# Kernel optimization log

Measured on AMD Instinct MI355X. Metric: run time of the kernel, lower is better.

## Reference

```python
import jax, jax.numpy as jnp
import numpy as np

DN = ('NCHW', 'OIHW', 'NCHW')
WINDOW_SIZES = (11, 25, 49)


def conv(x, w, b=None, pad=0, groups=1):
    y = jax.lax.conv_general_dilated(
        x, w, window_strides=(1, 1), padding=((pad, pad), (pad, pad)),
        dimension_numbers=DN, feature_group_count=groups)
    if b is not None:
        y = y + b[None, :, None, None]
    return y


def box_mean(f, wsize):
    # depthwise box-filter local mean with reflect padding (matches F.pad mode='reflect')
    C = f.shape[1]
    p = wsize // 2
    fp = jnp.pad(f, ((0, 0), (0, 0), (p, p), (p, p)), mode='reflect')
    k = jnp.ones((C, 1, wsize, wsize), f.dtype) / (wsize * wsize)
    return conv(fp, k, groups=C)


def std_map(features, wsize):
    # per-channel local std, channel-weighted sum, then **0.8
    C = features.shape[1]
    # C == 8 here, so weights are softmax(ones) == uniform (torch path for C != 4)
    cw = jax.nn.softmax(jnp.ones((C,), features.dtype))
    m = box_mean(features, wsize)
    m2 = box_mean(features ** 2, wsize)
    var = jnp.clip(m2 - m ** 2, 1e-6, None)
    res = jnp.sum(cw[None, :, None, None] * jnp.sqrt(var), axis=1, keepdims=True)
    return res ** 0.8  # [B,1,H,W]


def setup_inputs() -> dict:
    key = jax.random.key(0)
    ks = jax.random.split(key, 8)
    B, C, H, W = 8, 4, 512, 512
    x = jax.random.normal(ks[0], (B, C, H, W), dtype=jnp.float32)
    conv1_w = jax.random.normal(ks[1], (32, 4, 3, 3), dtype=jnp.float32) * 0.1
    conv1_b = jnp.zeros((32,), jnp.float32)
    conv2_w = jax.random.normal(ks[2], (16, 32, 3, 3), dtype=jnp.float32) * 0.05
    conv2_b = jnp.zeros((16,), jnp.float32)
    conv3_w = jax.random.normal(ks[3], (8, 16, 3, 3), dtype=jnp.float32) * 0.05
    conv3_b = jnp.zeros((8,), jnp.float32)
    # scale_fusion init: weight = 1/len(window_sizes), bias = 0
    fusion_w = jnp.full((1, len(WINDOW_SIZES), 1, 1), 1.0 / len(WINDOW_SIZES), jnp.float32)
    fusion_b = jnp.zeros((1,), jnp.float32)
    channel_weights = jnp.ones((4,), jnp.float32) / 4.0
    return dict(x=x, conv1_w=conv1_w, conv1_b=conv1_b, conv2_w=conv2_w,
                conv2_b=conv2_b, conv3_w=conv3_w, conv3_b=conv3_b,
                fusion_w=fusion_w, fusion_b=fusion_b,
                channel_weights=channel_weights)


def reference(x, conv1_w, conv1_b, conv2_w, conv2_b, conv3_w, conv3_b,
              fusion_w, fusion_b, channel_weights):
    lrelu = lambda v: jnp.where(v >= 0, v, 0.2 * v)
    # feature extractor: conv3x3 -> lrelu -> conv3x3 -> lrelu -> conv3x3
    f = lrelu(conv(x, conv1_w, conv1_b, pad=1))
    f = lrelu(conv(f, conv2_w, conv2_b, pad=1))
    f = conv(f, conv3_w, conv3_b, pad=1)  # [B,8,H,W]
    # multi-scale std maps
    maps = [std_map(f, w) for w in WINDOW_SIZES]
    multi = jnp.concatenate(maps, axis=1)  # [B,3,H,W]
    fused = jax.nn.relu(conv(multi, fusion_w, fusion_b, pad=0))  # [B,1,H,W]
    # adaptive thresholds (global quantiles over the whole fused std map)
    qs = jnp.quantile(fused.reshape(-1), jnp.array([0.25, 0.75], fused.dtype))
    q25, q75 = qs[0], qs[1]
    iqr = q75 - q25
    gstd = jnp.std(x, axis=(2, 3), keepdims=True, ddof=1)  # [B,4,1,1] (torch unbiased)
    lo = (q25 - 0.5 * iqr) * jnp.ones_like(gstd)
    hi = (q75 + 0.5 * iqr) * jnp.ones_like(gstd)
    gf = jnp.clip(gstd * 5.0, 0.5, 2.0)
    lo, hi = lo * gf, hi * gf
    cw = jax.nn.softmax(channel_weights)[None, :, None, None]
    cstd = jnp.std(x * cw, axis=(2, 3), keepdims=True, ddof=1)
    cf = jnp.clip(cstd * 2.0, 0.8, 1.2)
    lo, hi = lo * cf, hi * cf
    # mask generation: broadcast [B,1,H,W] vs [B,4,1,1] -> [B,4,H,W], then mean over C
    n = jnp.clip((fused - lo) / (hi - lo), 0.0, 1.0)
    mask = jax.nn.sigmoid(6.0 * n - 3.0)
    return jnp.mean(mask, axis=1, keepdims=True)  # [B,1,H,W]
```

## Files before the change

kernel.cpp:

```cpp
#include <hip/hip_runtime.h>
#include <cmath>

#define HH 512
#define WW 512
#define NB 8
#define CIN 4
#define C2 32
#define C3 16
#define CF 8
#define HW (HH*WW)
#define NPIX (NB*HW)
#define NBC 2

#define SEGC 10
#define SW   320
#define SVW  ((SW + (SW>>4) + 3) | 1)
#define RSW  (256 + 16 + 2)

__device__ __forceinline__ float lrelu_f(float v){ return v < 0.f ? 0.2f*v : v; }
__device__ __forceinline__ int reflect_i(int i){ int r = i < 0 ? -i : i; return r >= HH ? 2*HH - 2 - r : r; }
__device__ __forceinline__ int swz(int j){ return j + (j >> 4); }

template<int Ci, int Co, bool LRELU>
__global__ __launch_bounds__(256) void k_conv8(const float* __restrict__ in,
                                               const float* __restrict__ wgt,
                                               const float* __restrict__ bias,
                                               float* __restrict__ outp)
{
    constexpr int NG = Co/8;
    __shared__ float wl[NG*Ci*72];
    __shared__ float bl[Co];
    for (int i = threadIdx.x; i < Co*Ci*9; i += 256){
        int g  = i / (Ci*72);
        int r  = i - g*(Ci*72);
        int ci = r / 72;
        int q  = r - ci*72;
        int tap = q >> 3, ocl = q & 7;
        wl[i] = wgt[((g*8 + ocl)*Ci + ci)*9 + tap];
    }
    if (threadIdx.x < Co) bl[threadIdx.x] = bias[threadIdx.x];
    __syncthreads();

    int bid   = blockIdx.x;
    int local = bid % (NG*128);
    int b     = bid / (NG*128);
    int cb    = local & 3;
    int rb    = (local >> 2) & 31;
    int cg    = local >> 7;
    int tid   = threadIdx.x;
    int lane  = tid & 31;
    int col   = cb*128 + lane*4;
    int row0  = rb*16  + (tid >> 5)*2;
    int co0   = cg*8;
    const float* inb = in + (size_t)b*Ci*HW;

    float acc[8][2][4];
    #pragma unroll
    for (int j=0;j<8;j++){
        float bv = bl[co0+j];
        #pragma unroll
        for (int r=0;r<2;r++)
            #pragma unroll
            for (int p=0;p<4;p++) acc[j][r][p] = bv;
    }

    #pragma unroll 1
    for (int ci=0; ci<Ci; ci++){
        float v[4][6];
        const float* inc = inb + (size_t)ci*HW;
        #pragma unroll
        for (int dy=0;dy<4;dy++){
            int hh = row0 + dy - 1;
            int hc = hh < 0 ? 0 : (hh > HH-1 ? HH-1 : hh);
            bool hok = (unsigned)hh < (unsigned)HH;
            const float* rowp = inc + hc*WW;
            float4 m  = *(const float4*)(rowp + col);
            float  v0 = (col > 0)      ? rowp[col-1] : 0.f;
            float  v5 = (col+4 < WW)   ? rowp[col+4] : 0.f;
            if (!hok){ m.x=0.f; m.y=0.f; m.z=0.f; m.w=0.f; v0=0.f; v5=0.f; }
            v[dy][0]=v0; v[dy][1]=m.x; v[dy][2]=m.y;
            v[dy][3]=m.z; v[dy][4]=m.w; v[dy][5]=v5;
        }
        const float* wp = &wl[(cg*Ci + ci)*72];
        #pragma unroll
        for (int t=0;t<9;t++){
            int dy = t/3, dx = t - 3*(t/3);
            float w8[8];
            #pragma unroll
            for (int o=0;o<8;o++) w8[o] = wp[t*8 + o];
            #pragma unroll
            for (int o=0;o<8;o++)
                #pragma unroll
                for (int r=0;r<2;r++)
                    #pragma unroll
                    for (int p=0;p<4;p++)
                        acc[o][r][p] = fmaf(v[dy+r][dx+p], w8[o], acc[o][r][p]);
        }
    }

    float* ob = outp + (size_t)b*Co*HW;
    #pragma unroll
    for (int j=0;j<8;j++){
        #pragma unroll
        for (int r=0;r<2;r++){
            float4 o;
            o.x = LRELU ? lrelu_f(acc[j][r][0]) : acc[j][r][0];
            o.y = LRELU ? lrelu_f(acc[j][r][1]) : acc[j][r][1];
            o.z = LRELU ? lrelu_f(acc[j][r][2]) : acc[j][r][2];
            o.w = LRELU ? lrelu_f(acc[j][r][3]) : acc[j][r][3];
            *(float4*)(ob + (size_t)(co0+j)*HW + (size_t)(row0+r)*WW + col) = o;
        }
    }
}

template<int WS>
__device__ __forceinline__ float scale_step(float2* __restrict__ svq,
                                            float* __restrict__ resv,
                                            const float* vs, const float* vq,
                                            float fws)
{
    constexpr int P   = WS/2;
    constexpr int OFF = 24 - P;
    constexpr float inv = 1.f/((float)WS*(float)WS);
    const int tid = threadIdx.x;
    const int ch  = tid >> 5;
    const int seg = tid & 31;

    __syncthreads();
    #pragma unroll
    for (int k=0;k<SEGC;k++){
        int j = k*32 + seg;
        svq[ch*SVW + swz(j)] = make_float2(vs[k], vq[k]);
    }
    __syncthreads();

    int base = OFF + seg*8;
    float S = 0.f, Q = 0.f;
    #pragma unroll
    for (int q=0;q<WS;q++){
        float2 t = svq[ch*SVW + swz(base+q)];
        S += t.x; Q += t.y;
    }
    float res[8];
    #pragma unroll
    for (int t8=0;t8<8;t8++){
        float m = S*inv, m2 = Q*inv;
        res[t8] = sqrtf(fmaxf(fmaf(-m, m, m2), 1e-6f));
        if (t8 < 7){
            float2 ta = svq[ch*SVW + swz(base+t8+WS)];
            float2 tb = svq[ch*SVW + swz(base+t8)];
            S += ta.x - tb.x; Q += ta.y - tb.y;
        }
    }
    #pragma unroll
    for (int t8=0;t8<8;t8++)
        resv[ch*RSW + swz(seg*8+t8)] = res[t8];
    __syncthreads();

    float a = 0.f;
    #pragma unroll
    for (int cc=0;cc<CF;cc++) a += resv[cc*RSW + swz(tid)];
    return fws * powf(a*0.125f, 0.8f);
}

__global__ __launch_bounds__(256) void k_std3(const float* __restrict__ f,
                                              float* __restrict__ fused,
                                              const float* __restrict__ fwv)
{
    __shared__ float2 svq[CF*SVW];
    __shared__ float  resv[CF*RSW];

    int bid  = blockIdx.x;
    int band = bid & 31;
    int half = (bid >> 5) & 1;
    int b    = bid >> 6;
    int r0   = band*16;
    int c0   = half*256;
    int tid  = threadIdx.x;
    int ch   = tid >> 5;
    int seg  = tid & 31;
    const float* fp = f + (size_t)(b*CF + ch)*HW;

    int rc[SEGC];
    #pragma unroll
    for (int k=0;k<SEGC;k++){
        int gc = c0 - 24 + k*32 + seg;
        gc = gc < 0 ? -gc : (gc > WW-1 ? 2*WW-2 - gc : gc);
        rc[k] = gc;
    }

    float vs49[SEGC], vq49[SEGC], vs25[SEGC], vq25[SEGC], vs11[SEGC], vq11[SEGC];
    #pragma unroll
    for (int k=0;k<SEGC;k++){
        vs49[k]=0.f; vq49[k]=0.f; vs25[k]=0.f; vq25[k]=0.f; vs11[k]=0.f; vq11[k]=0.f;
    }
    #pragma unroll 1
    for (int dy=-24; dy<=24; dy++){
        const float* rp = fp + (size_t)reflect_i(r0+dy)*WW;
        bool in25 = (dy >= -12 && dy <= 12);
        bool in11 = (dy >= -5  && dy <= 5);
        #pragma unroll
        for (int k=0;k<SEGC;k++){
            float v = rp[rc[k]]; float v2 = v*v;
            vs49[k] += v; vq49[k] += v2;
            if (in25){ vs25[k] += v; vq25[k] += v2; }
            if (in11){ vs11[k] += v; vq11[k] += v2; }
        }
    }

    float fw0 = fwv[0], fw1 = fwv[1], fw2 = fwv[2];

    for (int rr=0; rr<16; rr++){
        int r = r0 + rr;
        float val;
        val  = scale_step<11>(svq, resv, vs11, vq11, fw0);
        val += scale_step<25>(svq, resv, vs25, vq25, fw1);
        val += scale_step<49>(svq, resv, vs49, vq49, fw2);
        fused[((size_t)b*HH + r)*WW + c0 + tid] = val;
        if (rr < 15){
            {   const float* ep = fp + (size_t)reflect_i(r+25)*WW;
                const float* lp = fp + (size_t)reflect_i(r-24)*WW;
                #pragma unroll
                for (int k=0;k<SEGC;k++){
                    float e = ep[rc[k]], l = lp[rc[k]];
                    vs49[k] += e - l;
                    vq49[k] = fmaf(e, e, vq49[k]); vq49[k] = fmaf(-l, l, vq49[k]);
                }
            }
            {   const float* ep = fp + (size_t)reflect_i(r+13)*WW;
                const float* lp = fp + (size_t)reflect_i(r-12)*WW;
                #pragma unroll
                for (int k=0;k<SEGC;k++){
                    float e = ep[rc[k]], l = lp[rc[k]];
                    vs25[k] += e - l;
                    vq25[k] = fmaf(e, e, vq25[k]); vq25[k] = fmaf(-l, l, vq25[k]);
                }
            }
            {   const float* ep = fp + (size_t)reflect_i(r+6)*WW;
                const float* lp = fp + (size_t)reflect_i(r-5)*WW;
                #pragma unroll
                for (int k=0;k<SEGC;k++){
                    float e = ep[rc[k]], l = lp[rc[k]];
                    vs11[k] += e - l;
                    vq11[k] = fmaf(e, e, vq11[k]); vq11[k] = fmaf(-l, l, vq11[k]);
                }
            }
        }
    }
}

__global__ void k_h8(const float* __restrict__ fused, const float* __restrict__ fb,
                     unsigned* __restrict__ hist8)
{
    __shared__ unsigned lh[256];
    lh[threadIdx.x] = 0;
    __syncthreads();
    float fbv = fb[0];
    int i = blockIdx.x*256 + threadIdx.x;
    int stride = gridDim.x*256;
    for (; i < NPIX; i += stride){
        float v = fmaxf(fused[i] + fbv, 0.f);
        atomicAdd(&lh[__float_as_uint(v) >> 24], 1u);
    }
    __syncthreads();
    if (lh[threadIdx.x]) atomicAdd(&hist8[threadIdx.x], lh[threadIdx.x]);
}

__global__ void k_scan8(const unsigned* __restrict__ hist8,
                        int* __restrict__ cand8, int* __restrict__ rank8)
{
    if (threadIdx.x == 0){
        const unsigned RK[4] = {524287u, 524288u, 1572863u, 1572864u};
        unsigned cum = 0; int qi = 0;
        for (int b = 0; b < 256 && qi < 4; b++){
            unsigned cnt = hist8[b];
            while (qi < 4 && RK[qi] < cum + cnt){
                cand8[qi] = b; rank8[qi] = (int)(RK[qi] - cum); qi++;
            }
            cum += cnt;
        }
    }
}

__global__ void k_h8b(const float* __restrict__ fused, const float* __restrict__ fb,
                      const int* __restrict__ cand8, unsigned* __restrict__ hist8b)
{
    __shared__ unsigned lh[1024];
    for (int i = threadIdx.x; i < 1024; i += 256) lh[i] = 0;
    __syncthreads();
    float fbv = fb[0];
    int c0 = cand8[0], c1 = cand8[1], c2 = cand8[2], c3 = cand8[3];
    bool d1 = (c1 != c0);
    bool d2 = (c2 != c0) && (c2 != c1);
    bool d3 = (c3 != c0) && (c3 != c1) && (c3 != c2);
    int i = blockIdx.x*256 + threadIdx.x;
    int stride = gridDim.x*256;
    for (; i < NPIX; i += stride){
        unsigned u = __float_as_uint(fmaxf(fused[i] + fbv, 0.f));
        int hi = (int)(u >> 24);
        unsigned mid = (u >> 16) & 0xffu;
        if (hi == c0)       atomicAdd(&lh[mid],       1u);
        if (d1 && hi == c1) atomicAdd(&lh[256u+mid],  1u);
        if (d2 && hi == c2) atomicAdd(&lh[512u+mid],  1u);
        if (d3 && hi == c3) atomicAdd(&lh[768u+mid],  1u);
    }
    __syncthreads();
    for (int i = threadIdx.x; i < 1024; i += 256)
        if (lh[i]) atomicAdd(&hist8b[i], lh[i]);
}

__global__ void k_scan8b(const unsigned* __restrict__ hist8b,
                         const int* __restrict__ cand8, const int* __restrict__ rank8,
                         int* __restrict__ cand16, int* __restrict__ rank16)
{
    int qi = threadIdx.x;
    if (qi < 4){
        int slot = qi;
        for (int j = 0; j < qi; j++) if (cand8[j] == cand8[qi]){ slot = j; break; }
        const unsigned* h = hist8b + slot*256;
        unsigned k = (unsigned)rank8[qi], cum = 0;
        for (int b = 0; b < 256; b++){
            unsigned cnt = h[b];
            if (cnt && k >= cum && k < cum + cnt){
                cand16[qi] = (cand8[qi] << 8) | b;
                rank16[qi] = (int)(k - cum);
            }
            cum += cnt;
        }
    }
}

__global__ void k_h16(const float* __restrict__ fused, const float* __restrict__ fb,
                      const int* __restrict__ cand16, unsigned* __restrict__ histlo)
{
    float fbv = fb[0];
    int c0 = cand16[0], c1 = cand16[1], c2 = cand16[2], c3 = cand16[3];
    bool d1 = (c1 != c0);
    bool d2 = (c2 != c0) && (c2 != c1);
    bool d3 = (c3 != c0) && (c3 != c1) && (c3 != c2);
    int i = blockIdx.x*256 + threadIdx.x;
    int stride = gridDim.x*256;
    for (; i < NPIX; i += stride){
        unsigned u = __float_as_uint(fmaxf(fused[i] + fbv, 0.f));
        int hi = (int)(u >> 16);
        unsigned lo = u & 0xffffu;
        if (hi == c0)       atomicAdd(&histlo[lo],           1u);
        if (d1 && hi == c1) atomicAdd(&histlo[65536u + lo],  1u);
        if (d2 && hi == c2) atomicAdd(&histlo[131072u + lo], 1u);
        if (d3 && hi == c3) atomicAdd(&histlo[196608u + lo], 1u);
    }
}

__global__ void k_scan16(const unsigned* __restrict__ histlo,
                         const int* __restrict__ cand16, const int* __restrict__ rank16,
                         float* __restrict__ ostat)
{
    int qi = blockIdx.x;
    int slot = qi;
    for (int j = 0; j < qi; j++) if (cand16[j] == cand16[qi]){ slot = j; break; }
    const unsigned* hist = histlo + (size_t)slot*65536;
    __shared__ unsigned csum[256];
    __shared__ unsigned cbase[256];
    int t = threadIdx.x;
    unsigned s = 0;
    for (int i = 0; i < 256; i++) s += hist[t*256 + i];
    csum[t] = s;
    __syncthreads();
    if (t == 0){ unsigned run = 0; for (int i = 0; i < 256; i++){ cbase[i] = run; run += csum[i]; } }
    __syncthreads();
    unsigned k = (unsigned)rank16[qi];
    unsigned cum = cbase[t];
    for (int i = 0; i < 256; i++){
        unsigned cnt = hist[t*256 + i];
        if (cnt && k >= cum && k < cum + cnt)
            ostat[qi] = __uint_as_float(((unsigned)cand16[qi] << 16) | (unsigned)(t*256 + i));
        cum += cnt;
    }
}

__global__ void k_gstd_part(const float* __restrict__ x, double* __restrict__ part)
{
    int bid = blockIdx.x;
    int plane = bid >> 3, chunk = bid & 7;
    const float4* p4 = (const float4*)(x + (size_t)plane*HW + (size_t)chunk*32768);
    int t = threadIdx.x;
    double s=0.0, s2=0.0;
    for (int k=0;k<32;k++){
        float4 v = p4[k*256 + t];
        s  += (double)v.x + (double)v.y + (double)v.z + (double)v.w;
        s2 += (double)v.x*v.x + (double)v.y*v.y + (double)v.z*v.z + (double)v.w*v.w;
    }
    __shared__ double rs[256], rq[256];
    rs[t]=s; rq[t]=s2; __syncthreads();
    for (int off=128; off>0; off>>=1){
        if (t<off){ rs[t]+=rs[t+off]; rq[t]+=rq[t+off]; }
        __syncthreads();
    }
    if (t==0){ part[bid*2]=rs[0]; part[bid*2+1]=rq[0]; }
}

__global__ void k_gstd_final(const double* __restrict__ part, float* __restrict__ gstd)
{
    int t = threadIdx.x;
    if (t < 32){
        double s=0.0, s2=0.0;
        for (int j=0;j<8;j++){ s += part[(t*8+j)*2]; s2 += part[(t*8+j)*2+1]; }
        const double N = 262144.0;
        double var = (s2 - s*s/N) / (N - 1.0);
        gstd[t] = (float)sqrt(var < 0.0 ? 0.0 : var);
    }
}

__global__ void k_finalize(const float* __restrict__ ostat, const float* __restrict__ gstd,
                           const float* __restrict__ cwin, float* __restrict__ lov, float* __restrict__ hiv)
{
    int t = threadIdx.x;
    if (t < 32){
        float q25 = ostat[0] + 0.75f*(ostat[1]-ostat[0]);
        float q75 = ostat[2] + 0.25f*(ostat[3]-ostat[2]);
        float iqr = q75 - q25;
        float lo_b = q25 - 0.5f*iqr, hi_b = q75 + 0.5f*iqr;
        int c = t & 3;
        float m = fmaxf(fmaxf(cwin[0],cwin[1]), fmaxf(cwin[2],cwin[3]));
        float e0 = expf(cwin[0]-m), e1 = expf(cwin[1]-m), e2 = expf(cwin[2]-m), e3 = expf(cwin[3]-m);
        float smc = expf(cwin[c]-m) / (e0+e1+e2+e3);
        float g  = gstd[t];
        float gf = fminf(fmaxf(g*5.f, 0.5f), 2.f);
        float cf = fminf(fmaxf(smc*g*2.f, 0.8f), 1.2f);
        lov[t] = lo_b*gf*cf;
        hiv[t] = hi_b*gf*cf;
    }
}

__global__ void k_mask(const float* __restrict__ fused_in, const float* __restrict__ fb,
                       const float* __restrict__ lov, const float* __restrict__ hiv,
                       float* __restrict__ outp)
{
    int i = blockIdx.x*256 + threadIdx.x;
    float F = fmaxf(fused_in[i] + fb[0], 0.f);
    int b = i >> 18;
    float o = 0.f;
    #pragma unroll
    for (int c=0;c<4;c++){
        float lo = lov[b*4+c], hi = hiv[b*4+c];
        float n = (F - lo) / (hi - lo);
        n = fminf(fmaxf(n, 0.f), 1.f);
        o += 1.f/(1.f + expf(3.f - 6.f*n));
    }
    outp[i] = 0.25f * o;
}

extern "C" void kernel_launch(void* const* d_in, const int* in_sizes, int n_in,
                              void* d_out, int out_size, void* d_ws, size_t ws_size,
                              hipStream_t stream)
{
    const float* x  = (const float*)d_in[0];
    const float* w1 = (const float*)d_in[1];
    const float* b1 = (const float*)d_in[2];
    const float* w2 = (const float*)d_in[3];
    const float* b2 = (const float*)d_in[4];
    const float* w3 = (const float*)d_in[5];
    const float* b3 = (const float*)d_in[6];
    const float* fw = (const float*)d_in[7];
    const float* fb = (const float*)d_in[8];
    const float* cw = (const float*)d_in[9];
    float* out = (float*)d_out;
    char* ws = (char*)d_ws;

    size_t off = 0;
    auto take = [&](size_t bytes)->size_t{ size_t o = off; off += (bytes + 255) & ~(size_t)255; return o; };
    size_t o_h8     = take(256*4);
    size_t o_h8b    = take(1024*4);
    size_t o_histlo = take((size_t)4*65536*4);
    size_t o_c8     = take(4*4);
    size_t o_r8     = take(4*4);
    size_t o_c16    = take(4*4);
    size_t o_r16    = take(4*4);
    size_t o_os     = take(4*4);
    size_t o_part   = take(512*8);
    size_t o_gs     = take(32*4);
    size_t o_lo     = take(32*4);
    size_t o_hi     = take(32*4);
    size_t o_R1     = take((size_t)NB*C3*HW*4);
    size_t o_R2     = take((size_t)NBC*C2*HW*4);

    float*    f2buf  = (float*)(ws + o_R1);
    float*    f1     = (float*)(ws + o_R2);
    float*    fbuf   = (float*)(ws + o_R2);
    unsigned* hist8  = (unsigned*)(ws + o_h8);
    unsigned* hist8b = (unsigned*)(ws + o_h8b);
    unsigned* histlo = (unsigned*)(ws + o_histlo);
    int*      c8     = (int*)(ws + o_c8);
    int*      r8     = (int*)(ws + o_r8);
    int*      c16    = (int*)(ws + o_c16);
    int*      r16    = (int*)(ws + o_r16);
    float*    osv    = (float*)(ws + o_os);
    double*   part   = (double*)(ws + o_part);
    float*    gs     = (float*)(ws + o_gs);
    float*    lov    = (float*)(ws + o_lo);
    float*    hiv    = (float*)(ws + o_hi);
    size_t hist_bytes = (o_histlo + (size_t)4*65536*4) - o_h8;

    for (int ck = 0; ck < NB/NBC; ck++){
        const float* xb = x + (size_t)ck*NBC*CIN*HW;
        k_conv8<CIN,C2,true ><<<NBC*512,256,0,stream>>>(xb, w1, b1, f1);
        k_conv8<C2, C3,true ><<<NBC*256,256,0,stream>>>(f1, w2, b2,
                                                        f2buf + (size_t)ck*NBC*C3*HW);
    }
    k_conv8<C3, CF, false><<<NB*128,256,0,stream>>>(f2buf, w3, b3, fbuf);

    k_gstd_part<<<256,256,0,stream>>>(x, part);
    k_gstd_final<<<1,256,0,stream>>>(part, gs);

    k_std3<<<NB*2*32,256,0,stream>>>(fbuf, out, fw);

    hipMemsetAsync(hist8, 0, hist_bytes, stream);
    k_h8    <<<2048,256,0,stream>>>(out, fb, hist8);
    k_scan8 <<<1,64,0,stream>>>(hist8, c8, r8);
    k_h8b   <<<2048,256,0,stream>>>(out, fb, c8, hist8b);
    k_scan8b<<<1,64,0,stream>>>(hist8b, c8, r8, c16, r16);
    k_h16   <<<2048,256,0,stream>>>(out, fb, c16, histlo);
    k_scan16<<<4,256,0,stream>>>(histlo, c16, r16, osv);

    k_finalize<<<1,64,0,stream>>>(osv, gs, cw, lov, hiv);
    k_mask<<<NPIX/256,256,0,stream>>>(out, fb, lov, hiv, out);
}
```

Before: 827.4 us.

## Fuse first histogram pass into std kernel and merge final small kernels

The first 8-bit radix histogram is now accumulated inside the std-map kernel, and the fused bias plus ReLU is applied there once. This removes a full read of the fused map and the bias re-application in the later histogram and mask kernels. The gstd-final, scan16 and finalize kernels are merged into one single-block kernel, which cuts launches. The conv ci-loop is unrolled by 2 for the first two convs with hoisted row offsets, and the shared-memory swizzle stride changes from 16 to 8. Shared-memory atomics in the std kernel may add contention, and the unrolled conv may raise register pressure.

```diff
diff --git a/kernel.cpp b/kernel.cpp
--- a/kernel.cpp
+++ b/kernel.cpp
@@ -14,14 +14,45 @@
 
 #define SEGC 10
 #define SW   320
-#define SVW  ((SW + (SW>>4) + 3) | 1)
-#define RSW  (256 + 16 + 2)
+#define SVW  ((SW + (SW>>3) + 4) | 1)
+#define RSW  (256 + 32 + 4)
 
 __device__ __forceinline__ float lrelu_f(float v){ return v < 0.f ? 0.2f*v : v; }
 __device__ __forceinline__ int reflect_i(int i){ int r = i < 0 ? -i : i; return r >= HH ? 2*HH - 2 - r : r; }
-__device__ __forceinline__ int swz(int j){ return j + (j >> 4); }
-
-template<int Ci, int Co, bool LRELU>
+__device__ __forceinline__ int swz(int j){ return j + (j >> 3); }
+
+#define CIBODY \
+    { \
+        const float* inc = inb + (size_t)ci*HW; \
+        float v[4][6]; \
+        _Pragma("unroll") \
+        for (int dy=0;dy<4;dy++){ \
+            const float* rowp = inc + hcofs[dy]; \
+            float4 mq = *(const float4*)(rowp + col); \
+            float v0 = (col > 0)    ? rowp[col-1] : 0.f; \
+            float v5 = (col+4 < WW) ? rowp[col+4] : 0.f; \
+            if (!hok[dy]){ mq.x=0.f; mq.y=0.f; mq.z=0.f; mq.w=0.f; v0=0.f; v5=0.f; } \
+            v[dy][0]=v0; v[dy][1]=mq.x; v[dy][2]=mq.y; \
+            v[dy][3]=mq.z; v[dy][4]=mq.w; v[dy][5]=v5; \
+        } \
+        const float* wp = &wl[(cg*Ci + ci)*72]; \
+        _Pragma("unroll") \
+        for (int t=0;t<9;t++){ \
+            int dy = t/3, dx = t - 3*(t/3); \
+            float w8[8]; \
+            _Pragma("unroll") \
+            for (int o=0;o<8;o++) w8[o] = wp[t*8 + o]; \
+            _Pragma("unroll") \
+            for (int o=0;o<8;o++) \
+                _Pragma("unroll") \
+                for (int r=0;r<2;r++) \
+                    _Pragma("unroll") \
+                    for (int p=0;p<4;p++) \
+                        acc[o][r][p] = fmaf(v[dy+r][dx+p], w8[o], acc[o][r][p]); \
+        } \
+    }
+
+template<int Ci, int Co, bool LRELU, bool UNR2>
 __global__ __launch_bounds__(256) void k_conv8(const float* __restrict__ in,
                                                const float* __restrict__ wgt,
                                                const float* __restrict__ bias,
@@ -54,6 +85,15 @@
     int co0   = cg*8;
     const float* inb = in + (size_t)b*Ci*HW;
 
+    int  hcofs[4]; bool hok[4];
+    #pragma unroll
+    for (int dy=0;dy<4;dy++){
+        int hh = row0 + dy - 1;
+        int hc = hh < 0 ? 0 : (hh > HH-1 ? HH-1 : hh);
+        hok[dy]   = (unsigned)hh < (unsigned)HH;
+        hcofs[dy] = hc*WW;
+    }
+
     float acc[8][2][4];
     #pragma unroll
     for (int j=0;j<8;j++){
@@ -64,38 +104,12 @@
             for (int p=0;p<4;p++) acc[j][r][p] = bv;
     }
 
-    #pragma unroll 1
-    for (int ci=0; ci<Ci; ci++){
-        float v[4][6];
-        const float* inc = inb + (size_t)ci*HW;
-        #pragma unroll
-        for (int dy=0;dy<4;dy++){
-            int hh = row0 + dy - 1;
-            int hc = hh < 0 ? 0 : (hh > HH-1 ? HH-1 : hh);
-            bool hok = (unsigned)hh < (unsigned)HH;
-            const float* rowp = inc + hc*WW;
-            float4 m  = *(const float4*)(rowp + col);
-            float  v0 = (col > 0)      ? rowp[col-1] : 0.f;
-            float  v5 = (col+4 < WW)   ? rowp[col+4] : 0.f;
-            if (!hok){ m.x=0.f; m.y=0.f; m.z=0.f; m.w=0.f; v0=0.f; v5=0.f; }
-            v[dy][0]=v0; v[dy][1]=m.x; v[dy][2]=m.y;
-            v[dy][3]=m.z; v[dy][4]=m.w; v[dy][5]=v5;
-        }
-        const float* wp = &wl[(cg*Ci + ci)*72];
-        #pragma unroll
-        for (int t=0;t<9;t++){
-            int dy = t/3, dx = t - 3*(t/3);
-            float w8[8];
-            #pragma unroll
-            for (int o=0;o<8;o++) w8[o] = wp[t*8 + o];
-            #pragma unroll
-            for (int o=0;o<8;o++)
-                #pragma unroll
-                for (int r=0;r<2;r++)
-                    #pragma unroll
-                    for (int p=0;p<4;p++)
-                        acc[o][r][p] = fmaf(v[dy+r][dx+p], w8[o], acc[o][r][p]);
-        }
+    if constexpr (UNR2){
+        #pragma unroll 2
+        for (int ci=0; ci<Ci; ci++) CIBODY
+    } else {
+        #pragma unroll 1
+        for (int ci=0; ci<Ci; ci++) CIBODY
     }
 
     float* ob = outp + (size_t)b*Co*HW;
@@ -165,10 +179,14 @@
 
 __global__ __launch_bounds__(256) void k_std3(const float* __restrict__ f,
                                               float* __restrict__ fused,
-                                              const float* __restrict__ fwv)
+                                              const float* __restrict__ fwv,
+                                              const float* __restrict__ fbp,
+                                              unsigned* __restrict__ hist8)
 {
     __shared__ float2 svq[CF*SVW];
     __shared__ float  resv[CF*RSW];
+    __shared__ unsigned lh8[256];
+    lh8[threadIdx.x] = 0;
 
     int bid  = blockIdx.x;
     int band = bid & 31;
@@ -209,6 +227,7 @@
     }
 
     float fw0 = fwv[0], fw1 = fwv[1], fw2 = fwv[2];
+    float fbv = fbp[0];
 
     for (int rr=0; rr<16; rr++){
         int r = r0 + rr;
@@ -216,7 +235,9 @@
         val  = scale_step<11>(svq, resv, vs11, vq11, fw0);
         val += scale_step<25>(svq, resv, vs25, vq25, fw1);
         val += scale_step<49>(svq, resv, vs49, vq49, fw2);
-        fused[((size_t)b*HH + r)*WW + c0 + tid] = val;
+        float F = fmaxf(val + fbv, 0.f);
+        fused[((size_t)b*HH + r)*WW + c0 + tid] = F;
+        atomicAdd(&lh8[__float_as_uint(F) >> 24], 1u);
         if (rr < 15){
             {   const float* ep = fp + (size_t)reflect_i(r+25)*WW;
                 const float* lp = fp + (size_t)reflect_i(r-24)*WW;
@@ -247,23 +268,8 @@
             }
         }
     }
-}
-
-__global__ void k_h8(const float* __restrict__ fused, const float* __restrict__ fb,
-                     unsigned* __restrict__ hist8)
-{
-    __shared__ unsigned lh[256];
-    lh[threadIdx.x] = 0;
-    __syncthreads();
-    float fbv = fb[0];
-    int i = blockIdx.x*256 + threadIdx.x;
-    int stride = gridDim.x*256;
-    for (; i < NPIX; i += stride){
-        float v = fmaxf(fused[i] + fbv, 0.f);
-        atomicAdd(&lh[__float_as_uint(v) >> 24], 1u);
-    }
-    __syncthreads();
-    if (lh[threadIdx.x]) atomicAdd(&hist8[threadIdx.x], lh[threadIdx.x]);
+    __syncthreads();
+    if (lh8[tid]) atomicAdd(&hist8[tid], lh8[tid]);
 }
 
 __global__ void k_scan8(const unsigned* __restrict__ hist8,
@@ -282,13 +288,12 @@
     }
 }
 
-__global__ void k_h8b(const float* __restrict__ fused, const float* __restrict__ fb,
+__global__ void k_h8b(const float* __restrict__ fused,
                       const int* __restrict__ cand8, unsigned* __restrict__ hist8b)
 {
     __shared__ unsigned lh[1024];
     for (int i = threadIdx.x; i < 1024; i += 256) lh[i] = 0;
     __syncthreads();
-    float fbv = fb[0];
     int c0 = cand8[0], c1 = cand8[1], c2 = cand8[2], c3 = cand8[3];
     bool d1 = (c1 != c0);
     bool d2 = (c2 != c0) && (c2 != c1);
@@ -296,7 +301,7 @@
     int i = blockIdx.x*256 + threadIdx.x;
     int stride = gridDim.x*256;
     for (; i < NPIX; i += stride){
-        unsigned u = __float_as_uint(fmaxf(fused[i] + fbv, 0.f));
+        unsigned u = __float_as_uint(fused[i]);
         int hi = (int)(u >> 24);
         unsigned mid = (u >> 16) & 0xffu;
         if (hi == c0)       atomicAdd(&lh[mid],       1u);
@@ -330,10 +335,9 @@
     }
 }
 
-__global__ void k_h16(const float* __restrict__ fused, const float* __restrict__ fb,
+__global__ void k_h16(const float* __restrict__ fused,
                       const int* __restrict__ cand16, unsigned* __restrict__ histlo)
 {
-    float fbv = fb[0];
     int c0 = cand16[0], c1 = cand16[1], c2 = cand16[2], c3 = cand16[3];
     bool d1 = (c1 != c0);
     bool d2 = (c2 != c0) && (c2 != c1);
@@ -341,40 +345,13 @@
     int i = blockIdx.x*256 + threadIdx.x;
     int stride = gridDim.x*256;
     for (; i < NPIX; i += stride){
-        unsigned u = __float_as_uint(fmaxf(fused[i] + fbv, 0.f));
+        unsigned u = __float_as_uint(fused[i]);
         int hi = (int)(u >> 16);
         unsigned lo = u & 0xffffu;
         if (hi == c0)       atomicAdd(&histlo[lo],           1u);
         if (d1 && hi == c1) atomicAdd(&histlo[65536u + lo],  1u);
         if (d2 && hi == c2) atomicAdd(&histlo[131072u + lo], 1u);
         if (d3 && hi == c3) atomicAdd(&histlo[196608u + lo], 1u);
-    }
-}
-
-__global__ void k_scan16(const unsigned* __restrict__ histlo,
-                         const int* __restrict__ cand16, const int* __restrict__ rank16,
-                         float* __restrict__ ostat)
-{
-    int qi = blockIdx.x;
-    int slot = qi;
-    for (int j = 0; j < qi; j++) if (cand16[j] == cand16[qi]){ slot = j; break; }
-    const unsigned* hist = histlo + (size_t)slot*65536;
-    __shared__ unsigned csum[256];
-    __shared__ unsigned cbase[256];
-    int t = threadIdx.x;
-    unsigned s = 0;
-    for (int i = 0; i < 256; i++) s += hist[t*256 + i];
-    csum[t] = s;
-    __syncthreads();
-    if (t == 0){ unsigned run = 0; for (int i = 0; i < 256; i++){ cbase[i] = run; run += csum[i]; } }
-    __syncthreads();
-    unsigned k = (unsigned)rank16[qi];
-    unsigned cum = cbase[t];
-    for (int i = 0; i < 256; i++){
-        unsigned cnt = hist[t*256 + i];
-        if (cnt && k >= cum && k < cum + cnt)
-            ostat[qi] = __uint_as_float(((unsigned)cand16[qi] << 16) | (unsigned)(t*256 + i));
-        cum += cnt;
     }
 }
 
@@ -399,32 +376,49 @@
     if (t==0){ part[bid*2]=rs[0]; part[bid*2+1]=rq[0]; }
 }
 
-__global__ void k_gstd_final(const double* __restrict__ part, float* __restrict__ gstd)
-{
+__global__ void k_fin(const unsigned* __restrict__ histlo,
+                      const int* __restrict__ cand16, const int* __restrict__ rank16,
+                      const double* __restrict__ part, const float* __restrict__ cwin,
+                      float* __restrict__ lov, float* __restrict__ hiv)
+{
+    __shared__ float ostat_s[4];
+    __shared__ unsigned csum[256];
+    __shared__ unsigned cbase[256];
     int t = threadIdx.x;
+    for (int qi = 0; qi < 4; qi++){
+        int slot = qi;
+        for (int j = 0; j < qi; j++) if (cand16[j] == cand16[qi]){ slot = j; break; }
+        const unsigned* hist = histlo + (size_t)slot*65536;
+        unsigned s = 0;
+        for (int i = 0; i < 256; i++) s += hist[t*256 + i];
+        csum[t] = s;
+        __syncthreads();
+        if (t == 0){ unsigned run = 0; for (int i = 0; i < 256; i++){ cbase[i] = run; run += csum[i]; } }
+        __syncthreads();
+        unsigned k = (unsigned)rank16[qi];
+        unsigned cum = cbase[t];
+        for (int i = 0; i < 256; i++){
+            unsigned cnt = hist[t*256 + i];
+            if (cnt && k >= cum && k < cum + cnt)
+                ostat_s[qi] = __uint_as_float(((unsigned)cand16[qi] << 16) | (unsigned)(t*256 + i));
+            cum += cnt;
+        }
+        __syncthreads();
+    }
     if (t < 32){
         double s=0.0, s2=0.0;
         for (int j=0;j<8;j++){ s += part[(t*8+j)*2]; s2 += part[(t*8+j)*2+1]; }
         const double N = 262144.0;
         double var = (s2 - s*s/N) / (N - 1.0);
-        gstd[t] = (float)sqrt(var < 0.0 ? 0.0 : var);
-    }
-}
-
-__global__ void k_finalize(const float* __restrict__ ostat, const float* __restrict__ gstd,
-                           const float* __restrict__ cwin, float* __restrict__ lov, float* __restrict__ hiv)
-{
-    int t = threadIdx.x;
-    if (t < 32){
-        float q25 = ostat[0] + 0.75f*(ostat[1]-ostat[0]);
-        float q75 = ostat[2] + 0.25f*(ostat[3]-ostat[2]);
+        float g = (float)sqrt(var < 0.0 ? 0.0 : var);
+        float q25 = ostat_s[0] + 0.75f*(ostat_s[1]-ostat_s[0]);
+        float q75 = ostat_s[2] + 0.25f*(ostat_s[3]-ostat_s[2]);
         float iqr = q75 - q25;
         float lo_b = q25 - 0.5f*iqr, hi_b = q75 + 0.5f*iqr;
         int c = t & 3;
         float m = fmaxf(fmaxf(cwin[0],cwin[1]), fmaxf(cwin[2],cwin[3]));
         float e0 = expf(cwin[0]-m), e1 = expf(cwin[1]-m), e2 = expf(cwin[2]-m), e3 = expf(cwin[3]-m);
         float smc = expf(cwin[c]-m) / (e0+e1+e2+e3);
-        float g  = gstd[t];
         float gf = fminf(fmaxf(g*5.f, 0.5f), 2.f);
         float cf = fminf(fmaxf(smc*g*2.f, 0.8f), 1.2f);
         lov[t] = lo_b*gf*cf;
@@ -432,12 +426,12 @@
     }
 }
 
-__global__ void k_mask(const float* __restrict__ fused_in, const float* __restrict__ fb,
+__global__ void k_mask(const float* __restrict__ fused_in,
                        const float* __restrict__ lov, const float* __restrict__ hiv,
                        float* __restrict__ outp)
 {
     int i = blockIdx.x*256 + threadIdx.x;
-    float F = fmaxf(fused_in[i] + fb[0], 0.f);
+    float F = fused_in[i];
     int b = i >> 18;
     float o = 0.f;
     #pragma unroll
@@ -476,9 +470,7 @@
     size_t o_r8     = take(4*4);
     size_t o_c16    = take(4*4);
     size_t o_r16    = take(4*4);
-    size_t o_os     = take(4*4);
     size_t o_part   = take(512*8);
-    size_t o_gs     = take(32*4);
     size_t o_lo     = take(32*4);
     size_t o_hi     = take(32*4);
     size_t o_R1     = take((size_t)NB*C3*HW*4);
@@ -494,34 +486,29 @@
     int*      r8     = (int*)(ws + o_r8);
     int*      c16    = (int*)(ws + o_c16);
     int*      r16    = (int*)(ws + o_r16);
-    float*    osv    = (float*)(ws + o_os);
     double*   part   = (double*)(ws + o_part);
-    float*    gs     = (float*)(ws + o_gs);
     float*    lov    = (float*)(ws + o_lo);
     float*    hiv    = (float*)(ws + o_hi);
     size_t hist_bytes = (o_histlo + (size_t)4*65536*4) - o_h8;
 
     for (int ck = 0; ck < NB/NBC; ck++){
         const float* xb = x + (size_t)ck*NBC*CIN*HW;
-        k_conv8<CIN,C2,true ><<<NBC*512,256,0,stream>>>(xb, w1, b1, f1);
-        k_conv8<C2, C3,true ><<<NBC*256,256,0,stream>>>(f1, w2, b2,
+        k_conv8<CIN,C2,true ,true ><<<NBC*512,256,0,stream>>>(xb, w1, b1, f1);
+        k_conv8<C2, C3,true ,true ><<<NBC*256,256,0,stream>>>(f1, w2, b2,
                                                         f2buf + (size_t)ck*NBC*C3*HW);
     }
-    k_conv8<C3, CF, false><<<NB*128,256,0,stream>>>(f2buf, w3, b3, fbuf);
+    k_conv8<C3, CF, false,false><<<NB*128,256,0,stream>>>(f2buf, w3, b3, fbuf);
 
     k_gstd_part<<<256,256,0,stream>>>(x, part);
-    k_gstd_final<<<1,256,0,stream>>>(part, gs);
-
-    k_std3<<<NB*2*32,256,0,stream>>>(fbuf, out, fw);
 
     hipMemsetAsync(hist8, 0, hist_bytes, stream);
-    k_h8    <<<2048,256,0,stream>>>(out, fb, hist8);
+    k_std3<<<NB*2*32,256,0,stream>>>(fbuf, out, fw, fb, hist8);
+
     k_scan8 <<<1,64,0,stream>>>(hist8, c8, r8);
-    k_h8b   <<<2048,256,0,stream>>>(out, fb, c8, hist8b);
+    k_h8b   <<<2048,256,0,stream>>>(out, c8, hist8b);
     k_scan8b<<<1,64,0,stream>>>(hist8b, c8, r8, c16, r16);
-    k_h16   <<<2048,256,0,stream>>>(out, fb, c16, histlo);
-    k_scan16<<<4,256,0,stream>>>(histlo, c16, r16, osv);
-
-    k_finalize<<<1,64,0,stream>>>(osv, gs, cw, lov, hiv);
-    k_mask<<<NPIX/256,256,0,stream>>>(out, fb, lov, hiv, out);
-}
+    k_h16   <<<2048,256,0,stream>>>(out, c16, histlo);
+    k_fin   <<<1,256,0,stream>>>(histlo, c16, r16, part, cw, lov, hiv);
+
+    k_mask<<<NPIX/256,256,0,stream>>>(out, lov, hiv, out);
+}
```

Measured after the change: 914.3 us. +10.5%, slower.
